# Kernel optimization log

Measured on AMD Instinct MI355X. Metric: run time of the kernel, lower is better.

## Reference

```python
import jax, jax.numpy as jnp
import numpy as np

B, N, F, FS, OUT, S, H, K = 1024, 256, 64, 128, 128, 4, 4, 4
EPS = 1e-5   # BatchNorm1d eps
BIG = 1e9    # sentinel distance for invalid nodes

# fully-connected segment edges (S nodes per graph, B graphs, flat node indexing)
_base = np.array([(i, j) for i in range(S) for j in range(S) if i != j], dtype=np.int32).T
_offs = (np.arange(B, dtype=np.int32) * S)[:, None]
CSRC = jnp.asarray((_base[0][None, :] + _offs).reshape(-1))
CDST = jnp.asarray((_base[1][None, :] + _offs).reshape(-1))
CMASK = jnp.ones(CSRC.shape[0], jnp.float32)


def _bn_relu(h, gamma, beta):
    # BatchNorm1d in training mode: biased batch statistics over the node axis
    mu = h.mean(0)
    var = jnp.var(h, axis=0)
    return jax.nn.relu((h - mu) * jax.lax.rsqrt(var + EPS) * gamma + beta)


def _graph_conv(x, src, dst, emask, W, b, gamma, beta):
    # linear -> gather(src) -> scatter-add(dst) -> degree norm -> BN -> ReLU
    h = x @ W + b
    agg = jax.ops.segment_sum(h[src] * emask[:, None], dst, num_segments=x.shape[0])
    deg = jnp.clip(jax.ops.segment_sum(emask, dst, num_segments=x.shape[0]), 1.0, None)
    return _bn_relu(h + agg / deg[:, None], gamma, beta)


def _knn_edges(positions, presence):
    # edges (i -> j) for each valid node i to its K nearest valid neighbors j
    valid = presence > 0.5                                    # [B,N]
    n_valid = valid.sum(-1)                                   # [B]
    diff = positions[:, :, None, :] - positions[:, None, :, :]
    d2 = jax.lax.stop_gradient(jnp.sum(diff * diff, -1))      # squared dist, same ordering as cdist
    d2 = jnp.where(valid[:, None, :], d2, BIG)                # mask invalid columns
    negv, idx = jax.lax.top_k(-d2, K + 1)                     # nearest first; idx[...,0] is self (dist 0)
    nbr, nd = idx[:, :, 1:], -negv[:, :, 1:]                  # [B,N,K]
    emask = valid[:, :, None] & (n_valid[:, None, None] >= 2) & (nd < 0.5 * BIG)
    offs = (jnp.arange(B) * N)[:, None, None]
    src = jnp.broadcast_to(jnp.arange(N)[None, :, None] + offs, (B, N, K)).reshape(-1)
    dst = jnp.where(emask, nbr + offs, 0).reshape(-1)
    return src, dst, emask.reshape(-1).astype(jnp.float32)


def setup_inputs() -> dict:
    key = jax.random.key(0)
    ks = jax.random.split(key, 16)
    rn = lambda k, shp, s=0.05: jax.random.normal(k, shp, jnp.float32) * s
    return {
        "axle_features": jax.random.normal(ks[0], (B, N, F), jnp.float32),
        "axle_positions": jax.random.normal(ks[1], (B, N, 2), jnp.float32),
        "presence_scores": jax.random.uniform(ks[2], (B, N), jnp.float32),
        "seg_queries": jax.random.normal(ks[3], (S, F), jnp.float32),
        "wq": rn(ks[4], (F, F)), "bq": jnp.zeros((F,), jnp.float32),
        "wk": rn(ks[5], (F, F)), "bk": jnp.zeros((F,), jnp.float32),
        "w_a2s": rn(ks[6], (F, FS)), "b_a2s": jnp.zeros((FS,), jnp.float32),
        "w_s2a": rn(ks[7], (FS, F)), "b_s2a": jnp.zeros((F,), jnp.float32),
        "coarse_W": rn(ks[8], (2, FS, FS)), "coarse_b": jnp.zeros((2, FS), jnp.float32),
        "coarse_gamma": jnp.ones((2, FS), jnp.float32), "coarse_beta": jnp.zeros((2, FS), jnp.float32),
        "fine_W": rn(ks[9], (3, F, F)), "fine_b": jnp.zeros((3, F), jnp.float32),
        "fine_gamma": jnp.ones((3, F), jnp.float32), "fine_beta": jnp.zeros((3, F), jnp.float32),
        "w_out": rn(ks[10], (F, OUT)), "b_out": jnp.zeros((OUT,), jnp.float32),
    }


def reference(axle_features, axle_positions, presence_scores, seg_queries, wq, bq, wk, bk,
              w_a2s, b_a2s, w_s2a, b_s2a, coarse_W, coarse_b, coarse_gamma, coarse_beta,
              fine_W, fine_b, fine_gamma, fine_beta, w_out, b_out):
    hd = F // H
    # LearnableSegmentation: MHA attention weights (head-averaged), then softmax over segments
    q = (seg_queries @ wq + bq).reshape(S, H, hd)
    k = (axle_features @ wk + bk).reshape(B, N, H, hd)
    scores = jnp.einsum('shd,bnhd->bhsn', q, k) / np.sqrt(hd)
    attn = jax.nn.softmax(scores, -1).mean(1)                 # [B,S,N]
    assign = jax.nn.softmax(jnp.swapaxes(attn, 1, 2), -1)     # [B,N,S]
    # segment pooling + coarse GNN over fully-connected segment graph
    proj = axle_features @ w_a2s + b_a2s                      # [B,N,FS]
    sf = jnp.einsum('bns,bnf->bsf', assign, proj).reshape(B * S, FS)
    for l in range(coarse_W.shape[0]):
        sf = _graph_conv(sf, CSRC, CDST, CMASK, coarse_W[l], coarse_b[l], coarse_gamma[l], coarse_beta[l])
    ctx = jnp.einsum('bns,bsf->bnf', assign, sf.reshape(B, S, FS)) @ w_s2a + b_s2a
    # fine GNN over kNN axle graph
    src, dst, em = _knn_edges(axle_positions, presence_scores)
    af = (axle_features + ctx).reshape(B * N, F)
    for l in range(fine_W.shape[0]):
        af = _graph_conv(af, src, dst, em, fine_W[l], fine_b[l], fine_gamma[l], fine_beta[l])
    # presence-weighted pooling + output projection
    pw = presence_scores[:, :, None]
    g = (af.reshape(B, N, F) * pw).sum(1) / jnp.clip(pw.sum(1), 1e-8, None)
    return g @ w_out + b_out
```

## Files before the change

kernel.cpp:

```cpp
#include <hip/hip_runtime.h>
#include <hip/hip_bf16.h>
#include <math.h>

#define BB   1024
#define NN   256
#define FF   64
#define FSS  128
#define OUTT 128
#define SS   4
#define HH   4
#define KK   4
#define HDD  16
#define EPSF 1e-5f
#define BIGF 1000000000.0f
#define ROWB 72

typedef __attribute__((ext_vector_type(8))) short short8;
typedef __attribute__((ext_vector_type(4))) float f32x4;

static __device__ __forceinline__ unsigned short f2bf(float f) {
  union { float f; unsigned u; } x; x.f = f;
  unsigned u = x.u + 0x7fffu + ((x.u >> 16) & 1u);
  return (unsigned short)(u >> 16);
}
static __device__ __forceinline__ float bf2f(unsigned short h) {
  union { unsigned u; float f; } x; x.u = ((unsigned)h) << 16;
  return x.f;
}

__global__ __launch_bounds__(256) void k_prep(
    const float* __restrict__ sq, const float* __restrict__ wq, const float* __restrict__ bq,
    const float* __restrict__ wk, const float* __restrict__ bk,
    float* __restrict__ V_o, float* __restrict__ c_o)
{
  const int tid = threadIdx.x;
  __shared__ float sq_s[SS*FF];
  __shared__ float q_s[SS*FF];
  sq_s[tid] = sq[tid];
  __syncthreads();
  {
    int s = tid >> 6, f = tid & 63;
    float acc = bq[f];
    for (int c = 0; c < FF; ++c) acc += sq_s[s*FF+c] * wq[c*FF+f];
    q_s[s*FF+f] = acc;
  }
  __syncthreads();
  {
    int c = tid & 63, jb = (tid >> 6) * 4;
    for (int jj = 0; jj < 4; ++jj) {
      int j = jb + jj, h = j >> 2, s = j & 3;
      float acc = 0.f;
      for (int d = 0; d < HDD; ++d)
        acc += wk[c*FF + h*HDD + d] * q_s[s*FF + h*HDD + d];
      V_o[c*16 + j] = acc * 0.25f;
    }
  }
  if (tid < 16) {
    int h = tid >> 2, s = tid & 3;
    float acc = 0.f;
    for (int d = 0; d < HDD; ++d) acc += bk[h*HDD+d] * q_s[s*FF + h*HDD + d];
    c_o[tid] = acc * 0.25f;
  }
}

__global__ __launch_bounds__(256, 2) void k_attn_sf(
    const float* __restrict__ axle,
    const float* __restrict__ Vm, const float* __restrict__ cv,
    const float* __restrict__ w_a2s, const float* __restrict__ b_a2s,
    float* __restrict__ assign_o, float* __restrict__ sf_o)
{
  const int b = blockIdx.x, tid = threadIdx.x;
  const int wv = tid >> 6, ln = tid & 63;
  __shared__ float x_s[NN*(FF+1)];
  __shared__ __align__(16) unsigned char u_buf[16*NN*2];
  __shared__ float mz_s[16][2];
  __hip_bfloat16* sc_s = (__hip_bfloat16*)u_buf;
  float (*as_s)[SS]    = (float (*)[SS])u_buf;
  float* t_s           = (float*)(u_buf + 4096);
  float* As_s          = (float*)(u_buf + 4096 + 1024);

  const float* afb = axle + (size_t)b*NN*FF;
  for (int i = tid; i < NN*FF; i += 256)
    x_s[(i>>6)*(FF+1) + (i&63)] = afb[i];
  __syncthreads();

  {
    float sc[16];
    #pragma unroll
    for (int j = 0; j < 16; ++j) sc[j] = cv[j];
    #pragma unroll
    for (int c = 0; c < FF; ++c) {
      float xc = x_s[tid*(FF+1)+c];
      #pragma unroll
      for (int j = 0; j < 16; ++j) sc[j] = fmaf(xc, Vm[c*16+j], sc[j]);
    }
    #pragma unroll
    for (int j = 0; j < 16; ++j) sc_s[j*NN + tid] = __float2bfloat16(sc[j]);
  }
  __syncthreads();

  for (int r = 0; r < 4; ++r) {
    int row = wv*4 + r;
    float v0 = __bfloat162float(sc_s[row*NN + ln]);
    float v1 = __bfloat162float(sc_s[row*NN + ln + 64]);
    float v2 = __bfloat162float(sc_s[row*NN + ln + 128]);
    float v3 = __bfloat162float(sc_s[row*NN + ln + 192]);
    float m = fmaxf(fmaxf(v0,v1), fmaxf(v2,v3));
    #pragma unroll
    for (int o = 32; o; o >>= 1) m = fmaxf(m, __shfl_xor(m, o));
    float z = __expf(v0-m) + __expf(v1-m) + __expf(v2-m) + __expf(v3-m);
    #pragma unroll
    for (int o = 32; o; o >>= 1) z += __shfl_xor(z, o);
    if (ln == 0) { mz_s[row][0] = m; mz_s[row][1] = 1.f/z; }
  }
  __syncthreads();

  float4 av;
  {
    float at0 = 0.f, at1 = 0.f, at2 = 0.f, at3 = 0.f;
    #pragma unroll
    for (int h = 0; h < HH; ++h) {
      at0 += __expf(__bfloat162float(sc_s[(h*4+0)*NN + tid]) - mz_s[h*4+0][0]) * mz_s[h*4+0][1];
      at1 += __expf(__bfloat162float(sc_s[(h*4+1)*NN + tid]) - mz_s[h*4+1][0]) * mz_s[h*4+1][1];
      at2 += __expf(__bfloat162float(sc_s[(h*4+2)*NN + tid]) - mz_s[h*4+2][0]) * mz_s[h*4+2][1];
      at3 += __expf(__bfloat162float(sc_s[(h*4+3)*NN + tid]) - mz_s[h*4+3][0]) * mz_s[h*4+3][1];
    }
    at0 *= 0.25f; at1 *= 0.25f; at2 *= 0.25f; at3 *= 0.25f;
    float m = fmaxf(fmaxf(at0,at1), fmaxf(at2,at3));
    float e0=__expf(at0-m), e1=__expf(at1-m), e2=__expf(at2-m), e3=__expf(at3-m);
    float zi = 1.f/(e0+e1+e2+e3);
    av = make_float4(e0*zi, e1*zi, e2*zi, e3*zi);
    reinterpret_cast<float4*>(assign_o)[(size_t)b*NN + tid] = av;
  }
  __syncthreads();
  *reinterpret_cast<float4*>(&as_s[tid][0]) = av;
  __syncthreads();

  {
    int s = tid >> 6, c = tid & 63;
    float ac0=0.f, ac1=0.f, ac2=0.f, ac3=0.f, aa0=0.f, aa1=0.f;
    for (int n = 0; n < NN; n += 4) {
      float a0 = as_s[n+0][s], a1 = as_s[n+1][s], a2 = as_s[n+2][s], a3 = as_s[n+3][s];
      ac0 = fmaf(a0, x_s[(n+0)*(FF+1)+c], ac0);
      ac1 = fmaf(a1, x_s[(n+1)*(FF+1)+c], ac1);
      ac2 = fmaf(a2, x_s[(n+2)*(FF+1)+c], ac2);
      ac3 = fmaf(a3, x_s[(n+3)*(FF+1)+c], ac3);
      aa0 += a0 + a1; aa1 += a2 + a3;
    }
    t_s[s*FF + c] = (ac0+ac1)+(ac2+ac3);
    if (c == 0) As_s[s] = aa0 + aa1;
  }
  __syncthreads();

  for (int o = tid; o < SS*FSS; o += 256) {
    int s = o >> 7, f = o & 127;
    float acc = As_s[s] * b_a2s[f];
    for (int c = 0; c < FF; ++c) acc += t_s[s*FF + c] * w_a2s[c*FSS+f];
    sf_o[((size_t)b*SS+s)*FSS+f] = acc;
  }
}

__global__ __launch_bounds__(128) void k_coarse(
    const float* __restrict__ in, const float* __restrict__ W, const float* __restrict__ bias,
    const float* __restrict__ pmu, const float* __restrict__ prstd,
    const float* __restrict__ pgamma, const float* __restrict__ pbeta, int applyBN,
    float* __restrict__ out, float* __restrict__ stat1, float* __restrict__ stat2)
{
  const int b = blockIdx.x, f = threadIdx.x;
  __shared__ float x_s[SS][FSS];
  #pragma unroll
  for (int i = 0; i < SS; ++i) {
    float v = in[((size_t)b*SS+i)*FSS + f];
    if (applyBN) v = fmaxf((v - pmu[f])*prstd[f]*pgamma[f] + pbeta[f], 0.f);
    x_s[i][f] = v;
  }
  __syncthreads();
  float h0 = bias[f], h1 = h0, h2 = h0, h3 = h0;
  for (int c = 0; c < FSS; ++c) {
    float w = W[c*FSS+f];
    h0 += x_s[0][c]*w; h1 += x_s[1][c]*w; h2 += x_s[2][c]*w; h3 += x_s[3][c]*w;
  }
  float s4 = h0+h1+h2+h3;
  const float inv3 = 1.f/3.f;
  float o0 = h0 + (s4-h0)*inv3;
  float o1 = h1 + (s4-h1)*inv3;
  float o2 = h2 + (s4-h2)*inv3;
  float o3 = h3 + (s4-h3)*inv3;
  size_t ob = (size_t)b*SS*FSS + f;
  out[ob] = o0; out[ob+FSS] = o1; out[ob+2*FSS] = o2; out[ob+3*FSS] = o3;
  stat1[(size_t)f*BB + b] = o0+o1+o2+o3;
  stat2[(size_t)f*BB + b] = o0*o0+o1*o1+o2*o2+o3*o3;
}

__global__ __launch_bounds__(256) void k_bnstats(
    const float* __restrict__ s1, const float* __restrict__ s2,
    float* __restrict__ mu, float* __restrict__ rstd, float invcnt)
{
  const int f = blockIdx.x, tid = threadIdx.x;
  float a = 0.f, q = 0.f;
  for (int j = tid; j < BB; j += 256) { a += s1[(size_t)f*BB+j]; q += s2[(size_t)f*BB+j]; }
  #pragma unroll
  for (int o = 32; o; o >>= 1) { a += __shfl_xor(a, o); q += __shfl_xor(q, o); }
  __shared__ float ra[4], rq[4];
  int wv = tid >> 6;
  if ((tid & 63) == 0) { ra[wv] = a; rq[wv] = q; }
  __syncthreads();
  if (tid == 0) {
    float s = ra[0]+ra[1]+ra[2]+ra[3], ss = rq[0]+rq[1]+rq[2]+rq[3];
    float m = s*invcnt; float v = ss*invcnt - m*m;
    mu[f] = m; rstd[f] = 1.f / sqrtf(v + EPSF);
  }
}

__global__ __launch_bounds__(256) void k_knn(
    const float* __restrict__ pos, const float* __restrict__ pres,
    int* __restrict__ rev_go, int* __restrict__ offs_go,
    float* __restrict__ ivd_o, float* __restrict__ bf_o)
{
  const int b = blockIdx.x, tid = threadIdx.x;
  const int ln = tid & 63, wv = tid >> 6;
  __shared__ float px[NN], py[NN];
  __shared__ int vld[NN];
  __shared__ int wcnt[4];
  __shared__ int nbr_s[NN*KK];
  __shared__ int cnti[NN], scn[NN], cur[NN];
  __shared__ __align__(16) int rev_s[NN*KK];
  float2 p = reinterpret_cast<const float2*>(pos)[(size_t)b*NN + tid];
  float pr = pres[(size_t)b*NN + tid];
  int v = pr > 0.5f ? 1 : 0;
  px[tid] = p.x; py[tid] = p.y; vld[tid] = v;
  cnti[tid] = 0; cur[tid] = 0;
  #pragma unroll
  for (int k = 0; k < KK; ++k) rev_s[tid*KK+k] = 0;
  int cnt = v;
  #pragma unroll
  for (int o = 32; o; o >>= 1) cnt += __shfl_xor(cnt, o);
  if (ln == 0) wcnt[wv] = cnt;
  __syncthreads();
  int nv = wcnt[0]+wcnt[1]+wcnt[2]+wcnt[3];

  float b0=3.4e38f, b1=b0, b2=b0, b3=b0, b4=b0;
  int   j0=0, j1=0, j2=0, j3=0, j4=0;
  float xi = p.x, yi = p.y;
  for (int j = 0; j < NN; ++j) {
    float dx = __fsub_rn(xi, px[j]);
    float dy = __fsub_rn(yi, py[j]);
    float d2 = __fadd_rn(__fmul_rn(dx,dx), __fmul_rn(dy,dy));
    if (!vld[j]) d2 = BIGF;
    if (d2 < b4) {
      b4 = d2; j4 = j;
      if (b4 < b3) { float t=b3; b3=b4; b4=t; int ti=j3; j3=j4; j4=ti; }
      if (b3 < b2) { float t=b2; b2=b3; b3=t; int ti=j2; j2=j3; j3=ti; }
      if (b2 < b1) { float t=b1; b1=b2; b2=t; int ti=j1; j1=j2; j2=ti; }
      if (b1 < b0) { float t=b0; b0=b1; b1=t; int ti=j0; j0=j1; j1=ti; }
    }
  }
  (void)j0;
  bool okrow = (v != 0) && (nv >= 2);
  int d0 = (okrow && b1 < 0.5f*BIGF) ? j1 : -1;
  int d1 = (okrow && b2 < 0.5f*BIGF) ? j2 : -1;
  int d2i= (okrow && b3 < 0.5f*BIGF) ? j3 : -1;
  int d3 = (okrow && b4 < 0.5f*BIGF) ? j4 : -1;
  nbr_s[tid*KK+0] = d0; nbr_s[tid*KK+1] = d1;
  nbr_s[tid*KK+2] = d2i; nbr_s[tid*KK+3] = d3;
  if (d0 >= 0) atomicAdd(&cnti[d0], 1);
  if (d1 >= 0) atomicAdd(&cnti[d1], 1);
  if (d2i>= 0) atomicAdd(&cnti[d2i],1);
  if (d3 >= 0) atomicAdd(&cnti[d3], 1);
  __syncthreads();

  scn[tid] = cnti[tid];
  __syncthreads();
  for (int d = 1; d < NN; d <<= 1) {
    int t = (tid >= d) ? scn[tid-d] : 0;
    __syncthreads();
    scn[tid] += t;
    __syncthreads();
  }
  #pragma unroll
  for (int k = 0; k < KK; ++k) {
    int d = nbr_s[tid*KK+k];
    if (d >= 0) {
      int pp = atomicAdd(&cur[d], 1);
      rev_s[scn[d] - cnti[d] + pp] = tid;
    }
  }
  __syncthreads();

  int start = scn[tid] - cnti[tid];
  offs_go[(size_t)b*(NN+1) + tid] = start;
  if (tid == NN-1) offs_go[(size_t)b*(NN+1) + NN] = scn[NN-1];
  float cf = (float)cnti[tid];
  ivd_o[(size_t)b*NN + tid] = 1.f / fmaxf(cf, 1.f);
  bf_o[(size_t)b*NN + tid]  = cnti[tid] > 0 ? 2.f : 1.f;
  reinterpret_cast<int4*>(rev_go)[(size_t)b*NN + tid] =
      *reinterpret_cast<int4*>(&rev_s[tid*KK]);
}

__global__ __launch_bounds__(256) void k_ctx(
    const float* __restrict__ axle, const float* __restrict__ hc1,
    const float* __restrict__ mu, const float* __restrict__ rstd,
    const float* __restrict__ gamma, const float* __restrict__ beta,
    const float* __restrict__ assign_i,
    const float* __restrict__ w_s2a, const float* __restrict__ b_s2a,
    float* __restrict__ af_o)
{
  const int b = blockIdx.x, tid = threadIdx.x;
  __shared__ float csf[SS][FSS];
  __shared__ float u_s[SS][FF];
  for (int i = tid; i < SS*FSS; i += 256) {
    int s = i >> 7, f = i & 127;
    float v = hc1[((size_t)b*SS+s)*FSS + f];
    csf[s][f] = fmaxf((v - mu[f])*rstd[f]*gamma[f] + beta[f], 0.f);
  }
  __syncthreads();
  {
    int s = tid >> 6, f = tid & 63;
    float acc = 0.f;
    for (int c = 0; c < FSS; ++c) acc += csf[s][c] * w_s2a[c*FF+f];
    u_s[s][f] = acc;
  }
  __syncthreads();
  const size_t gb = (size_t)b*NN*FF;
  for (int i = tid; i < NN*FF; i += 256) {
    int n = i >> 6, f = i & 63;
    const float* ag = assign_i + ((size_t)b*NN + n)*SS;
    float acc = axle[gb+i] + b_s2a[f]
              + ag[0]*u_s[0][f] + ag[1]*u_s[1][f] + ag[2]*u_s[2][f] + ag[3]*u_s[3][f];
    af_o[gb+i] = acc;
  }
}

__global__ __launch_bounds__(512, 4) void k_fine3(
    float* __restrict__ af,
    const float* __restrict__ W, const float* __restrict__ bias,
    const float* __restrict__ pmu, const float* __restrict__ prstd,
    const float* __restrict__ pgamma, const float* __restrict__ pbeta, int applyBN,
    const int* __restrict__ rev_g, const int* __restrict__ offs_g,
    const float* __restrict__ ivd_g, const float* __restrict__ bf_g,
    float* __restrict__ stat1, float* __restrict__ stat2)
{
  const int b = blockIdx.x, tid = threadIdx.x;
  const int wv = tid >> 6, ln = tid & 63;
  const int l15 = ln & 15, g = ln >> 4;
  __shared__ __align__(16) unsigned short xb[NN*ROWB];
  __shared__ __align__(16) unsigned short wt[FF*ROWB];
  __shared__ int rev_s[NN*KK];
  __shared__ int offs_s[NN+1];
  __shared__ float ivd_s[NN], bf_s[NN];
  __shared__ float scale_s[FF], shift_s[FF];
  __shared__ float red1[8*FF], red2[8*FF];

  if (tid < FF) {
    if (applyBN) {
      float sc = prstd[tid]*pgamma[tid];
      scale_s[tid] = sc; shift_s[tid] = pbeta[tid] - pmu[tid]*sc;
    } else { scale_s[tid] = 1.f; shift_s[tid] = 0.f; }
  }
  for (int i = tid; i < NN*KK; i += 512) rev_s[i] = rev_g[(size_t)b*NN*KK + i];
  if (tid <= NN) offs_s[tid] = offs_g[(size_t)b*(NN+1) + tid];
  if (tid < NN) { ivd_s[tid] = ivd_g[(size_t)b*NN + tid]; bf_s[tid] = bf_g[(size_t)b*NN + tid]; }

  {
    const int c = tid >> 3, f0 = (tid & 7) * 8;
    float4 w0 = *reinterpret_cast<const float4*>(&W[c*FF + f0]);
    float4 w1 = *reinterpret_cast<const float4*>(&W[c*FF + f0 + 4]);
    wt[(f0+0)*ROWB + c] = f2bf(w0.x);
    wt[(f0+1)*ROWB + c] = f2bf(w0.y);
    wt[(f0+2)*ROWB + c] = f2bf(w0.z);
    wt[(f0+3)*ROWB + c] = f2bf(w0.w);
    wt[(f0+4)*ROWB + c] = f2bf(w1.x);
    wt[(f0+5)*ROWB + c] = f2bf(w1.y);
    wt[(f0+6)*ROWB + c] = f2bf(w1.z);
    wt[(f0+7)*ROWB + c] = f2bf(w1.w);
  }

  float* afb = af + (size_t)b*NN*FF;
  const float4* in4 = reinterpret_cast<const float4*>(afb);
  __syncthreads();

  for (int i4 = tid; i4 < NN*FF/4; i4 += 512) {
    float4 v = in4[i4];
    int c4 = (i4 & 15) * 4, n = i4 >> 4;
    v.x = v.x*scale_s[c4+0] + shift_s[c4+0];
    v.y = v.y*scale_s[c4+1] + shift_s[c4+1];
    v.z = v.z*scale_s[c4+2] + shift_s[c4+2];
    v.w = v.w*scale_s[c4+3] + shift_s[c4+3];
    if (applyBN) { v.x=fmaxf(v.x,0.f); v.y=fmaxf(v.y,0.f); v.z=fmaxf(v.z,0.f); v.w=fmaxf(v.w,0.f); }
    uint2 pk;
    pk.x = (unsigned)f2bf(v.x) | ((unsigned)f2bf(v.y) << 16);
    pk.y = (unsigned)f2bf(v.z) | ((unsigned)f2bf(v.w) << 16);
    *reinterpret_cast<uint2*>(&xb[n*ROWB + c4]) = pk;
  }
  __syncthreads();

  const int nb = wv << 5;
#define GATH(J) float y##J; { const int n_ = nb + (J); \
    const int s0_ = offs_s[n_]; const int s1_ = offs_s[n_+1]; \
    float sum_ = 0.f; \
    for (int i_ = s0_; i_ < s1_; ++i_) sum_ += bf2f(xb[rev_s[i_]*ROWB + ln]); \
    y##J = bf2f(xb[n_*ROWB + ln]) + ivd_s[n_]*sum_; }
  GATH(0)  GATH(1)  GATH(2)  GATH(3)  GATH(4)  GATH(5)  GATH(6)  GATH(7)
  GATH(8)  GATH(9)  GATH(10) GATH(11) GATH(12) GATH(13) GATH(14) GATH(15)
  GATH(16) GATH(17) GATH(18) GATH(19) GATH(20) GATH(21) GATH(22) GATH(23)
  GATH(24) GATH(25) GATH(26) GATH(27) GATH(28) GATH(29) GATH(30) GATH(31)
#undef GATH
  __syncthreads();
#define WRB(J) xb[(nb + (J))*ROWB + ln] = f2bf(y##J);
  WRB(0)  WRB(1)  WRB(2)  WRB(3)  WRB(4)  WRB(5)  WRB(6)  WRB(7)
  WRB(8)  WRB(9)  WRB(10) WRB(11) WRB(12) WRB(13) WRB(14) WRB(15)
  WRB(16) WRB(17) WRB(18) WRB(19) WRB(20) WRB(21) WRB(22) WRB(23)
  WRB(24) WRB(25) WRB(26) WRB(27) WRB(28) WRB(29) WRB(30) WRB(31)
#undef WRB
  __syncthreads();

  short8 areg[2][2], breg[4][2];
  #pragma unroll
  for (int rt2 = 0; rt2 < 2; ++rt2)
    #pragma unroll
    for (int ks = 0; ks < 2; ++ks)
      areg[rt2][ks] = *reinterpret_cast<const short8*>(
          &xb[((2*wv+rt2)*16 + l15)*ROWB + ks*32 + g*8]);
  #pragma unroll
  for (int ct = 0; ct < 4; ++ct)
    #pragma unroll
    for (int ks = 0; ks < 2; ++ks)
      breg[ct][ks] = *reinterpret_cast<const short8*>(
          &wt[(ct*16 + l15)*ROWB + ks*32 + g*8]);

  f32x4 acc[2][4];
  #pragma unroll
  for (int rt2 = 0; rt2 < 2; ++rt2)
    #pragma unroll
    for (int ct = 0; ct < 4; ++ct)
      acc[rt2][ct] = (f32x4){0.f, 0.f, 0.f, 0.f};
  #pragma unroll
  for (int rt2 = 0; rt2 < 2; ++rt2)
    #pragma unroll
    for (int ct = 0; ct < 4; ++ct)
      #pragma unroll
      for (int ks = 0; ks < 2; ++ks)
        acc[rt2][ct] = __builtin_amdgcn_mfma_f32_16x16x32_bf16(
            areg[rt2][ks], breg[ct][ks], acc[rt2][ct], 0, 0, 0);

  float bias_c[4];
  #pragma unroll
  for (int ct = 0; ct < 4; ++ct) bias_c[ct] = bias[ct*16 + l15];
  float ps[4] = {0.f,0.f,0.f,0.f}, pss[4] = {0.f,0.f,0.f,0.f};
  #pragma unroll
  for (int rt2 = 0; rt2 < 2; ++rt2) {
    #pragma unroll
    for (int i = 0; i < 4; ++i) {
      int row = (2*wv+rt2)*16 + g*4 + i;
      float bfr = bf_s[row];
      #pragma unroll
      for (int ct = 0; ct < 4; ++ct) {
        float o = acc[rt2][ct][i] + bfr*bias_c[ct];
        afb[row*FF + ct*16 + l15] = o;
        ps[ct] += o; pss[ct] += o*o;
      }
    }
  }
  #pragma unroll
  for (int ct = 0; ct < 4; ++ct) {
    float p = ps[ct], q = pss[ct];
    p += __shfl_xor(p, 16); p += __shfl_xor(p, 32);
    q += __shfl_xor(q, 16); q += __shfl_xor(q, 32);
    if (g == 0) { red1[wv*FF + ct*16 + l15] = p; red2[wv*FF + ct*16 + l15] = q; }
  }
  __syncthreads();
  if (tid < FF) {
    float s = 0.f, ss = 0.f;
    #pragma unroll
    for (int w = 0; w < 8; ++w) { s += red1[w*FF + tid]; ss += red2[w*FF + tid]; }
    stat1[(size_t)tid*BB + b] = s;
    stat2[(size_t)tid*BB + b] = ss;
  }
}

__global__ __launch_bounds__(256) void k_pool(
    const float* __restrict__ af, const float* __restrict__ pres,
    const float* __restrict__ pmu, const float* __restrict__ prstd,
    const float* __restrict__ pgamma, const float* __restrict__ pbeta,
    const float* __restrict__ w_out, const float* __restrict__ b_out,
    float* __restrict__ out)
{
  const int b = blockIdx.x, tid = threadIdx.x;
  const int wv = tid >> 6, ln = tid & 63;
  __shared__ float g_s[FF];
  __shared__ float red1[4][FF];
  __shared__ float pr_s[4];
  float pw = pres[(size_t)b*NN + tid];
  float t = pw;
  #pragma unroll
  for (int o = 32; o; o >>= 1) t += __shfl_xor(t, o);
  if (ln == 0) pr_s[wv] = t;
  float ps = 0.f;
  const size_t gb = (size_t)b*NN*FF;
  for (int i = tid; i < NN*FF; i += 256) {
    int n = i >> 6, f = i & 63;
    float v = af[gb+i];
    v = fmaxf((v - pmu[f])*prstd[f]*pgamma[f] + pbeta[f], 0.f);
    ps += v * pres[(size_t)b*NN + n];
  }
  red1[wv][ln] = ps;
  __syncthreads();
  if (tid < FF) {
    float s = red1[0][tid]+red1[1][tid]+red1[2][tid]+red1[3][tid];
    float den = fmaxf(pr_s[0]+pr_s[1]+pr_s[2]+pr_s[3], 1e-8f);
    g_s[tid] = s / den;
  }
  __syncthreads();
  if (tid < OUTT) {
    float acc = b_out[tid];
    for (int f = 0; f < FF; ++f) acc += g_s[f] * w_out[f*OUTT + tid];
    out[(size_t)b*OUTT + tid] = acc;
  }
}

extern "C" void kernel_launch(void* const* d_in, const int* in_sizes, int n_in,
                              void* d_out, int out_size, void* d_ws, size_t ws_size,
                              hipStream_t stream) {
  (void)in_sizes; (void)n_in; (void)out_size; (void)ws_size;
  const float* axle  = (const float*)d_in[0];
  const float* pos   = (const float*)d_in[1];
  const float* pres  = (const float*)d_in[2];
  const float* sq    = (const float*)d_in[3];
  const float* wq    = (const float*)d_in[4];
  const float* bq    = (const float*)d_in[5];
  const float* wk    = (const float*)d_in[6];
  const float* bk    = (const float*)d_in[7];
  const float* w_a2s = (const float*)d_in[8];
  const float* b_a2s = (const float*)d_in[9];
  const float* w_s2a = (const float*)d_in[10];
  const float* b_s2a = (const float*)d_in[11];
  const float* cW    = (const float*)d_in[12];
  const float* cb    = (const float*)d_in[13];
  const float* cg    = (const float*)d_in[14];
  const float* cbe   = (const float*)d_in[15];
  const float* fW    = (const float*)d_in[16];
  const float* fb    = (const float*)d_in[17];
  const float* fg    = (const float*)d_in[18];
  const float* fbe   = (const float*)d_in[19];
  const float* wout  = (const float*)d_in[20];
  const float* bout  = (const float*)d_in[21];
  float* out = (float*)d_out;

  char* base = (char*)d_ws;
  size_t off = 0;
  auto alloc = [&](size_t nbytes) -> void* {
    void* p = base + off; off += (nbytes + 255) & ~(size_t)255; return p;
  };
  float* af     = (float*)alloc((size_t)BB*NN*FF*4);
  float* assign = (float*)alloc((size_t)BB*NN*SS*4);
  float* sf     = (float*)alloc((size_t)BB*SS*FSS*4);
  float* hc0    = (float*)alloc((size_t)BB*SS*FSS*4);
  float* hc1    = (float*)alloc((size_t)BB*SS*FSS*4);
  int*   rev    = (int*)  alloc((size_t)BB*NN*KK*4);
  int*   offs   = (int*)  alloc((size_t)BB*(NN+1)*4);
  float* ivd    = (float*)alloc((size_t)BB*NN*4);
  float* bff    = (float*)alloc((size_t)BB*NN*4);
  float* st1    = (float*)alloc((size_t)FSS*BB*4);
  float* st2    = (float*)alloc((size_t)FSS*BB*4);
  float* mu0    = (float*)alloc(FSS*4);
  float* rs0    = (float*)alloc(FSS*4);
  float* mu1    = (float*)alloc(FSS*4);
  float* rs1    = (float*)alloc(FSS*4);
  float* muF    = (float*)alloc(FF*4);
  float* rsF    = (float*)alloc(FF*4);
  float* Vm     = (float*)alloc(FF*16*4);
  float* cv     = (float*)alloc(16*4);

  k_prep<<<1, 256, 0, stream>>>(sq, wq, bq, wk, bk, Vm, cv);
  k_attn_sf<<<BB, 256, 0, stream>>>(axle, Vm, cv, w_a2s, b_a2s, assign, sf);

  k_coarse<<<BB, 128, 0, stream>>>(sf,  cW,          cb,     mu0, rs0, cg, cbe, 0, hc0, st1, st2);
  k_bnstats<<<FSS, 256, 0, stream>>>(st1, st2, mu0, rs0, 1.f/((float)BB*SS));
  k_coarse<<<BB, 128, 0, stream>>>(hc0, cW+FSS*FSS,  cb+FSS, mu0, rs0, cg, cbe, 1, hc1, st1, st2);
  k_bnstats<<<FSS, 256, 0, stream>>>(st1, st2, mu1, rs1, 1.f/((float)BB*SS));

  k_knn<<<BB, 256, 0, stream>>>(pos, pres, rev, offs, ivd, bff);

  k_ctx<<<BB, 256, 0, stream>>>(axle, hc1, mu1, rs1, cg+FSS, cbe+FSS, assign, w_s2a, b_s2a, af);

  k_fine3<<<BB, 512, 0, stream>>>(af, fW,         fb,      muF, rsF, fg,    fbe,    0, rev, offs, ivd, bff, st1, st2);
  k_bnstats<<<FF, 256, 0, stream>>>(st1, st2, muF, rsF, 1.f/((float)BB*NN));
  k_fine3<<<BB, 512, 0, stream>>>(af, fW+FF*FF,   fb+FF,   muF, rsF, fg,    fbe,    1, rev, offs, ivd, bff, st1, st2);
  k_bnstats<<<FF, 256, 0, stream>>>(st1, st2, muF, rsF, 1.f/((float)BB*NN));
  k_fine3<<<BB, 512, 0, stream>>>(af, fW+2*FF*FF, fb+2*FF, muF, rsF, fg+FF, fbe+FF, 1, rev, offs, ivd, bff, st1, st2);
  k_bnstats<<<FF, 256, 0, stream>>>(st1, st2, muF, rsF, 1.f/((float)BB*NN));

  k_pool<<<BB, 256, 0, stream>>>(af, pres, muF, rsF, fg+2*FF, fbe+2*FF, wout, bout, out);
}
```

Baseline: 320.1 us.

## Store fine-GNN activations in bf16 and shrink attention LDS footprint

The intermediate fine-graph activation buffer changes from fp32 to bf16 across k_ctx, k_fine3 and k_pool, which halves its global memory traffic per layer. k_attn_sf now keeps the axle tile in LDS as packed bf16 instead of padded fp32, and occupancy hints are raised. k_fine3 reuses rev_s as its reduction scratch to cut LDS and allow more resident blocks. The cost is extra rounding of activations and of the attention input to bf16, which can shift accuracy.

```diff
diff --git a/kernel.cpp b/kernel.cpp
--- a/kernel.cpp
+++ b/kernel.cpp
@@ -14,6 +14,7 @@
 #define EPSF 1e-5f
 #define BIGF 1000000000.0f
 #define ROWB 72
+#define ROWA 68
 
 typedef __attribute__((ext_vector_type(8))) short short8;
 typedef __attribute__((ext_vector_type(4))) float f32x4;
@@ -26,6 +27,15 @@
 static __device__ __forceinline__ float bf2f(unsigned short h) {
   union { unsigned u; float f; } x; x.u = ((unsigned)h) << 16;
   return x.f;
+}
+static __device__ __forceinline__ float bflo(unsigned u) {
+  union { unsigned u; float f; } x; x.u = u << 16; return x.f;
+}
+static __device__ __forceinline__ float bfhi(unsigned u) {
+  union { unsigned u; float f; } x; x.u = u & 0xffff0000u; return x.f;
+}
+static __device__ __forceinline__ unsigned pack2(float a, float b) {
+  return (unsigned)f2bf(a) | ((unsigned)f2bf(b) << 16);
 }
 
 __global__ __launch_bounds__(256) void k_prep(
@@ -63,7 +73,7 @@
   }
 }
 
-__global__ __launch_bounds__(256, 2) void k_attn_sf(
+__global__ __launch_bounds__(256, 3) void k_attn_sf(
     const float* __restrict__ axle,
     const float* __restrict__ Vm, const float* __restrict__ cv,
     const float* __restrict__ w_a2s, const float* __restrict__ b_a2s,
@@ -71,7 +81,7 @@
 {
   const int b = blockIdx.x, tid = threadIdx.x;
   const int wv = tid >> 6, ln = tid & 63;
-  __shared__ float x_s[NN*(FF+1)];
+  __shared__ __align__(16) unsigned short xb_a[NN*ROWA];
   __shared__ __align__(16) unsigned char u_buf[16*NN*2];
   __shared__ float mz_s[16][2];
   __hip_bfloat16* sc_s = (__hip_bfloat16*)u_buf;
@@ -80,8 +90,13 @@
   float* As_s          = (float*)(u_buf + 4096 + 1024);
 
   const float* afb = axle + (size_t)b*NN*FF;
-  for (int i = tid; i < NN*FF; i += 256)
-    x_s[(i>>6)*(FF+1) + (i&63)] = afb[i];
+  const float4* in4 = reinterpret_cast<const float4*>(afb);
+  for (int i4 = tid; i4 < NN*FF/4; i4 += 256) {
+    float4 v = in4[i4];
+    int n = i4 >> 4, c4 = (i4 & 15) * 4;
+    uint2 pk; pk.x = pack2(v.x, v.y); pk.y = pack2(v.z, v.w);
+    *reinterpret_cast<uint2*>(&xb_a[n*ROWA + c4]) = pk;
+  }
   __syncthreads();
 
   {
@@ -89,10 +104,16 @@
     #pragma unroll
     for (int j = 0; j < 16; ++j) sc[j] = cv[j];
     #pragma unroll
-    for (int c = 0; c < FF; ++c) {
-      float xc = x_s[tid*(FF+1)+c];
+    for (int k = 0; k < 16; ++k) {
+      uint2 pk = *reinterpret_cast<const uint2*>(&xb_a[tid*ROWA + 4*k]);
+      float x0 = bflo(pk.x), x1 = bfhi(pk.x), x2 = bflo(pk.y), x3 = bfhi(pk.y);
       #pragma unroll
-      for (int j = 0; j < 16; ++j) sc[j] = fmaf(xc, Vm[c*16+j], sc[j]);
+      for (int j = 0; j < 16; ++j) {
+        float a = fmaf(x0, Vm[(4*k+0)*16+j], sc[j]);
+        a = fmaf(x1, Vm[(4*k+1)*16+j], a);
+        a = fmaf(x2, Vm[(4*k+2)*16+j], a);
+        sc[j] = fmaf(x3, Vm[(4*k+3)*16+j], a);
+      }
     }
     #pragma unroll
     for (int j = 0; j < 16; ++j) sc_s[j*NN + tid] = __float2bfloat16(sc[j]);
@@ -137,18 +158,24 @@
   __syncthreads();
 
   {
-    int s = tid >> 6, c = tid & 63;
-    float ac0=0.f, ac1=0.f, ac2=0.f, ac3=0.f, aa0=0.f, aa1=0.f;
-    for (int n = 0; n < NN; n += 4) {
-      float a0 = as_s[n+0][s], a1 = as_s[n+1][s], a2 = as_s[n+2][s], a3 = as_s[n+3][s];
-      ac0 = fmaf(a0, x_s[(n+0)*(FF+1)+c], ac0);
-      ac1 = fmaf(a1, x_s[(n+1)*(FF+1)+c], ac1);
-      ac2 = fmaf(a2, x_s[(n+2)*(FF+1)+c], ac2);
-      ac3 = fmaf(a3, x_s[(n+3)*(FF+1)+c], ac3);
-      aa0 += a0 + a1; aa1 += a2 + a3;
-    }
-    t_s[s*FF + c] = (ac0+ac1)+(ac2+ac3);
-    if (c == 0) As_s[s] = aa0 + aa1;
+    int s = wv, half = ln >> 5, c2 = ln & 31;
+    float t0 = 0.f, t1 = 0.f, aa = 0.f;
+    int n0 = half * 128;
+    for (int n = n0; n < n0 + 128; ++n) {
+      float a = as_s[n][s];
+      unsigned pk = *reinterpret_cast<const unsigned*>(&xb_a[n*ROWA + 2*c2]);
+      t0 = fmaf(a, bflo(pk), t0);
+      t1 = fmaf(a, bfhi(pk), t1);
+      aa += a;
+    }
+    t0 += __shfl_xor(t0, 32);
+    t1 += __shfl_xor(t1, 32);
+    aa += __shfl_xor(aa, 32);
+    if (half == 0) {
+      t_s[s*FF + 2*c2]     = t0;
+      t_s[s*FF + 2*c2 + 1] = t1;
+      if (c2 == 0) As_s[s] = aa;
+    }
   }
   __syncthreads();
 
@@ -303,7 +330,7 @@
     const float* __restrict__ gamma, const float* __restrict__ beta,
     const float* __restrict__ assign_i,
     const float* __restrict__ w_s2a, const float* __restrict__ b_s2a,
-    float* __restrict__ af_o)
+    unsigned short* __restrict__ af_o)
 {
   const int b = blockIdx.x, tid = threadIdx.x;
   __shared__ float csf[SS][FSS];
@@ -322,17 +349,23 @@
   }
   __syncthreads();
   const size_t gb = (size_t)b*NN*FF;
-  for (int i = tid; i < NN*FF; i += 256) {
-    int n = i >> 6, f = i & 63;
-    const float* ag = assign_i + ((size_t)b*NN + n)*SS;
-    float acc = axle[gb+i] + b_s2a[f]
-              + ag[0]*u_s[0][f] + ag[1]*u_s[1][f] + ag[2]*u_s[2][f] + ag[3]*u_s[3][f];
-    af_o[gb+i] = acc;
-  }
-}
-
-__global__ __launch_bounds__(512, 4) void k_fine3(
-    float* __restrict__ af,
+  const float4* ax4 = reinterpret_cast<const float4*>(axle + gb);
+  uint2* out2 = reinterpret_cast<uint2*>(af_o + gb);
+  for (int i4 = tid; i4 < NN*FF/4; i4 += 256) {
+    int n = i4 >> 4, c4 = (i4 & 15) * 4;
+    float4 ax = ax4[i4];
+    float4 ag = reinterpret_cast<const float4*>(assign_i)[(size_t)b*NN + n];
+    float o0 = ax.x + b_s2a[c4+0] + ag.x*u_s[0][c4+0] + ag.y*u_s[1][c4+0] + ag.z*u_s[2][c4+0] + ag.w*u_s[3][c4+0];
+    float o1 = ax.y + b_s2a[c4+1] + ag.x*u_s[0][c4+1] + ag.y*u_s[1][c4+1] + ag.z*u_s[2][c4+1] + ag.w*u_s[3][c4+1];
+    float o2 = ax.z + b_s2a[c4+2] + ag.x*u_s[0][c4+2] + ag.y*u_s[1][c4+2] + ag.z*u_s[2][c4+2] + ag.w*u_s[3][c4+2];
+    float o3 = ax.w + b_s2a[c4+3] + ag.x*u_s[0][c4+3] + ag.y*u_s[1][c4+3] + ag.z*u_s[2][c4+3] + ag.w*u_s[3][c4+3];
+    uint2 pk; pk.x = pack2(o0, o1); pk.y = pack2(o2, o3);
+    out2[i4] = pk;
+  }
+}
+
+__global__ __launch_bounds__(512, 6) void k_fine3(
+    unsigned short* __restrict__ af,
     const float* __restrict__ W, const float* __restrict__ bias,
     const float* __restrict__ pmu, const float* __restrict__ prstd,
     const float* __restrict__ pgamma, const float* __restrict__ pbeta, int applyBN,
@@ -345,11 +378,12 @@
   const int l15 = ln & 15, g = ln >> 4;
   __shared__ __align__(16) unsigned short xb[NN*ROWB];
   __shared__ __align__(16) unsigned short wt[FF*ROWB];
-  __shared__ int rev_s[NN*KK];
+  __shared__ __align__(16) int rev_s[NN*KK];
   __shared__ int offs_s[NN+1];
   __shared__ float ivd_s[NN], bf_s[NN];
   __shared__ float scale_s[FF], shift_s[FF];
-  __shared__ float red1[8*FF], red2[8*FF];
+  float* red1 = (float*)rev_s;
+  float* red2 = red1 + 8*FF;
 
   if (tid < FF) {
     if (applyBN) {
@@ -375,22 +409,31 @@
     wt[(f0+7)*ROWB + c] = f2bf(w1.w);
   }
 
-  float* afb = af + (size_t)b*NN*FF;
-  const float4* in4 = reinterpret_cast<const float4*>(afb);
-  __syncthreads();
-
-  for (int i4 = tid; i4 < NN*FF/4; i4 += 512) {
-    float4 v = in4[i4];
-    int c4 = (i4 & 15) * 4, n = i4 >> 4;
-    v.x = v.x*scale_s[c4+0] + shift_s[c4+0];
-    v.y = v.y*scale_s[c4+1] + shift_s[c4+1];
-    v.z = v.z*scale_s[c4+2] + shift_s[c4+2];
-    v.w = v.w*scale_s[c4+3] + shift_s[c4+3];
-    if (applyBN) { v.x=fmaxf(v.x,0.f); v.y=fmaxf(v.y,0.f); v.z=fmaxf(v.z,0.f); v.w=fmaxf(v.w,0.f); }
-    uint2 pk;
-    pk.x = (unsigned)f2bf(v.x) | ((unsigned)f2bf(v.y) << 16);
-    pk.y = (unsigned)f2bf(v.z) | ((unsigned)f2bf(v.w) << 16);
-    *reinterpret_cast<uint2*>(&xb[n*ROWB + c4]) = pk;
+  unsigned short* afb = af + (size_t)b*NN*FF;
+  const uint4* in8 = reinterpret_cast<const uint4*>(afb);
+  __syncthreads();
+
+  for (int i8 = tid; i8 < NN*FF/8; i8 += 512) {
+    uint4 raw = in8[i8];
+    int n = i8 >> 3, c8 = (i8 & 7) * 8;
+    float v0 = bflo(raw.x), v1 = bfhi(raw.x), v2 = bflo(raw.y), v3 = bfhi(raw.y);
+    float v4 = bflo(raw.z), v5 = bfhi(raw.z), v6 = bflo(raw.w), v7 = bfhi(raw.w);
+    v0 = v0*scale_s[c8+0] + shift_s[c8+0];
+    v1 = v1*scale_s[c8+1] + shift_s[c8+1];
+    v2 = v2*scale_s[c8+2] + shift_s[c8+2];
+    v3 = v3*scale_s[c8+3] + shift_s[c8+3];
+    v4 = v4*scale_s[c8+4] + shift_s[c8+4];
+    v5 = v5*scale_s[c8+5] + shift_s[c8+5];
+    v6 = v6*scale_s[c8+6] + shift_s[c8+6];
+    v7 = v7*scale_s[c8+7] + shift_s[c8+7];
+    if (applyBN) {
+      v0=fmaxf(v0,0.f); v1=fmaxf(v1,0.f); v2=fmaxf(v2,0.f); v3=fmaxf(v3,0.f);
+      v4=fmaxf(v4,0.f); v5=fmaxf(v5,0.f); v6=fmaxf(v6,0.f); v7=fmaxf(v7,0.f);
+    }
+    uint4 pk;
+    pk.x = pack2(v0, v1); pk.y = pack2(v2, v3);
+    pk.z = pack2(v4, v5); pk.w = pack2(v6, v7);
+    *reinterpret_cast<uint4*>(&xb[n*ROWB + c8]) = pk;
   }
   __syncthreads();
 
@@ -456,7 +499,7 @@
       #pragma unroll
       for (int ct = 0; ct < 4; ++ct) {
         float o = acc[rt2][ct][i] + bfr*bias_c[ct];
-        afb[row*FF + ct*16 + l15] = o;
+        afb[row*FF + ct*16 + l15] = f2bf(o);
         ps[ct] += o; pss[ct] += o*o;
       }
     }
@@ -479,7 +522,7 @@
 }
 
 __global__ __launch_bounds__(256) void k_pool(
-    const float* __restrict__ af, const float* __restrict__ pres,
+    const unsigned short* __restrict__ af, const float* __restrict__ pres,
     const float* __restrict__ pmu, const float* __restrict__ prstd,
     const float* __restrict__ pgamma, const float* __restrict__ pbeta,
     const float* __restrict__ w_out, const float* __restrict__ b_out,
@@ -499,7 +542,7 @@
   const size_t gb = (size_t)b*NN*FF;
   for (int i = tid; i < NN*FF; i += 256) {
     int n = i >> 6, f = i & 63;
-    float v = af[gb+i];
+    float v = bf2f(af[gb+i]);
     v = fmaxf((v - pmu[f])*prstd[f]*pgamma[f] + pbeta[f], 0.f);
     ps += v * pres[(size_t)b*NN + n];
   }
@@ -551,7 +594,7 @@
   auto alloc = [&](size_t nbytes) -> void* {
     void* p = base + off; off += (nbytes + 255) & ~(size_t)255; return p;
   };
-  float* af     = (float*)alloc((size_t)BB*NN*FF*4);
+  unsigned short* af = (unsigned short*)alloc((size_t)BB*NN*FF*2);
   float* assign = (float*)alloc((size_t)BB*NN*SS*4);
   float* sf     = (float*)alloc((size_t)BB*SS*FSS*4);
   float* hc0    = (float*)alloc((size_t)BB*SS*FSS*4);
```

After: 346.7 us. 8.3% more time.
